# Kernel tuning notes

Hardware: AMD Instinct MI355X
Metric: run time of the kernel (lower is better)

Reference implementation:

```python
import jax, jax.numpy as jnp
import numpy as np

NUM_HEADS = 4

def setup_inputs() -> dict:
    key = jax.random.key(0)
    ks = jax.random.split(key, 5)
    B, N, C = 2, 4096, 256
    s = 0.02
    return {
        "x": jax.random.normal(ks[0], (B, N, C), dtype=jnp.float32),
        "qkv_w": jax.random.normal(ks[1], (3 * C, C), dtype=jnp.float32) * s,
        "qkv_b": jax.random.normal(ks[2], (3 * C,), dtype=jnp.float32) * s,
        "out_w": jax.random.normal(ks[3], (C, C), dtype=jnp.float32) * s,
        "out_b": jax.random.normal(ks[4], (C,), dtype=jnp.float32) * s,
    }

def reference(x, qkv_w, qkv_b, out_w, out_b):
    # x: [B, N, C]; manual multi-head self-attention (eval mode, dropout off)
    B, N, C = x.shape
    H = NUM_HEADS
    D = C // H
    qkv = x @ qkv_w.T + qkv_b                      # [B, N, 3C]
    qkv = qkv.reshape(B, N, 3, H, D)
    qkv = jnp.transpose(qkv, (2, 0, 3, 1, 4))      # [3, B, H, N, D]
    q, k, v = qkv[0], qkv[1], qkv[2]
    scale = D ** -0.5
    attn = jnp.einsum('bhnd,bhmd->bhnm', q, k) * scale  # [B, H, N, N]
    attn = jax.nn.softmax(attn, axis=-1)
    out = jnp.einsum('bhnm,bhmd->bhnd', attn, v)   # [B, H, N, D]
    out = jnp.transpose(out, (0, 2, 1, 3)).reshape(B, N, C)
    return out @ out_w.T + out_b
```

## Files before the change

kernel.cpp:

```cpp
#include <hip/hip_runtime.h>

typedef __bf16 bf16x8 __attribute__((ext_vector_type(8)));
typedef float f32x4 __attribute__((ext_vector_type(4)));

#define MFMA_BF16(a, b, c) __builtin_amdgcn_mfma_f32_16x16x32_bf16((a), (b), (c), 0, 0, 0)

#define C1 0.18033688f

static __device__ __forceinline__ unsigned short f2bf(float f) {
    unsigned int u = __float_as_uint(f);
    unsigned int r = (u + 0x7fffu + ((u >> 16) & 1u)) >> 16;
    return (unsigned short)r;
}
static __device__ __forceinline__ float bf2f(unsigned short us) {
    return __uint_as_float(((unsigned int)us) << 16);
}
static __device__ __forceinline__ float exp2_hw(float x) {
    float r;
    asm("v_exp_f32 %0, %1" : "=v"(r) : "v"(x));
    return r;
}
static __device__ __forceinline__ unsigned pack_rh(float a, float b) {
    return __byte_perm(__float_as_uint(a) + 0x8000u, __float_as_uint(b) + 0x8000u, 0x7632);
}
static __device__ __forceinline__ void gload16(const void* g, void* l) {
    __builtin_amdgcn_global_load_lds(
        (const __attribute__((address_space(1))) unsigned int*)g,
        (__attribute__((address_space(3))) unsigned int*)l, 16, 0, 0);
}

static __device__ __forceinline__ void conv_seg8(const void* src, unsigned short* dst, int n,
                                                 int lb, bool f32) {
    const int base = lb * 2048 + (int)threadIdx.x * 8;
    if (base < n) {
        if (f32) {
            const float4 u0 = *(const float4*)((const float*)src + base);
            const float4 u1 = *(const float4*)((const float*)src + base + 4);
            uint4 p;
            p.x = pack_rh(u0.x, u0.y);
            p.y = pack_rh(u0.z, u0.w);
            p.z = pack_rh(u1.x, u1.y);
            p.w = pack_rh(u1.z, u1.w);
            *(uint4*)(dst + base) = p;
        } else {
            *(uint4*)(dst + base) = *(const uint4*)((const unsigned short*)src + base);
        }
    }
}

__global__ __launch_bounds__(256) void convert_kernel(
    const void* __restrict__ x, const void* __restrict__ qw, const void* __restrict__ qb,
    const void* __restrict__ ow, const void* __restrict__ ob,
    unsigned short* __restrict__ xb, unsigned short* __restrict__ qwb,
    unsigned short* __restrict__ qbb, unsigned short* __restrict__ owb,
    unsigned short* __restrict__ obb, int* __restrict__ flag) {
    __shared__ int tot;
    if (threadIdx.x == 0) tot = 0;
    __syncthreads();
    {
        unsigned short v = ((const unsigned short*)x)[threadIdx.x];
        int e = (v >> 7) & 0xFF;
        if (e >= 195) atomicAdd(&tot, 1);
    }
    __syncthreads();
    const bool f32 = (tot >= 8);
    if (blockIdx.x == 0 && threadIdx.x == 0) flag[0] = f32 ? 1 : 0;

    const int bid = blockIdx.x;
    if (bid < 1024)       conv_seg8(x,  xb,  2097152, bid,        f32);
    else if (bid < 1120)  conv_seg8(qw, qwb, 196608,  bid - 1024, f32);
    else if (bid < 1121)  conv_seg8(qb, qbb, 768,     bid - 1120, f32);
    else if (bid < 1153)  conv_seg8(ow, owb, 65536,   bid - 1121, f32);
    else                  conv_seg8(ob, obb, 256,     bid - 1153, f32);
}

template <bool QKV>
__global__ __launch_bounds__(256) void gemm_kernel(
    const unsigned short* __restrict__ A, const unsigned short* __restrict__ W,
    const unsigned short* __restrict__ bias, unsigned short* __restrict__ Cb,
    float* __restrict__ Cf, const int* __restrict__ flag,
    unsigned short* __restrict__ Vt, int Nout) {
    constexpr int K = 256;
    __shared__ __align__(16) char sm[16384];

    const int tid = threadIdx.x;
    const int lane = tid & 63;
    const int wv = tid >> 6;
    const int m16 = lane & 15;
    const int quad = lane >> 4;
    const int bm = blockIdx.x * 64;
    const int bn = blockIdx.y * 64;

    int bgo[2], blo[2];
#pragma unroll
    for (int i = 0; i < 2; i++) {
        const int c = wv * 128 + i * 64 + lane;
        const int r = c >> 3, g = (c & 7) ^ (r & 7);
        bgo[i] = r * (K * 2) + g * 16;
        blo[i] = c * 16;
    }
    int bro[4][2];
#pragma unroll
    for (int t = 0; t < 4; t++)
#pragma unroll
        for (int ks = 0; ks < 2; ks++) {
            const int row = t * 16 + m16;
            bro[t][ks] = row * 64 + ((4 * ks + quad) ^ (m16 & 7)) * 8;
        }

    const char* bg = (const char*)(W + (size_t)bn * K);
    const unsigned short* ap = A + (size_t)(bm + wv * 16 + m16) * K + quad * 8;

#pragma unroll
    for (int i = 0; i < 2; i++) gload16(bg + bgo[i], sm + blo[i]);
    bf16x8 a0 = *(const bf16x8*)(ap);
    bf16x8 a1 = *(const bf16x8*)(ap + 32);

    f32x4 acc[4] = {};
#pragma unroll
    for (int kb = 0; kb < 4; kb++) {
        __syncthreads();
        const int cur = kb & 1;
        bf16x8 a0n, a1n;
        if (kb < 3) {
            bg += 128;
            char* Bdst = sm + (cur ^ 1) * 8192;
#pragma unroll
            for (int i = 0; i < 2; i++) gload16(bg + bgo[i], Bdst + blo[i]);
            a0n = *(const bf16x8*)(ap + (kb + 1) * 64);
            a1n = *(const bf16x8*)(ap + (kb + 1) * 64 + 32);
        }
        const unsigned short* Blds = (const unsigned short*)(sm + cur * 8192);
#pragma unroll
        for (int ks = 0; ks < 2; ks++) {
            const bf16x8 a = ks ? a1 : a0;
#pragma unroll
            for (int t = 0; t < 4; t++) {
                const bf16x8 b = *(const bf16x8*)(Blds + bro[t][ks]);
                acc[t] = MFMA_BF16(a, b, acc[t]);
            }
        }
        if (kb < 3) {
            a0 = a0n;
            a1 = a1n;
        }
    }

    if (QKV && bn >= 512) {
        __syncthreads();
        unsigned short* tr = (unsigned short*)sm;
        const int lr = wv * 16 + quad * 4;
#pragma unroll
        for (int t = 0; t < 4; t++) {
            const float bv = bf2f(bias[bn + t * 16 + m16]);
            uint2 w;
            w.x = pack_rh(acc[t][0] + bv, acc[t][1] + bv);
            w.y = pack_rh(acc[t][2] + bv, acc[t][3] + bv);
            *(uint2*)&tr[(t * 16 + m16) * 72 + lr] = w;
        }
        __syncthreads();
        const int d = tid >> 2;
        const int ch = (tid & 3) * 16;
        const uint4 o4a = *(const uint4*)&tr[d * 72 + ch];
        const uint4 o4b = *(const uint4*)&tr[d * 72 + ch + 8];
        const int hh = (bn - 512) >> 6;
        const int bb = bm >> 12, n0 = bm & 4095;
        const int nn = n0 + ch;
        const int kt = nn >> 7, koff = nn & 127;
        unsigned short* vdst =
            &Vt[(size_t)(((bb * 4 + hh) * 32 + kt) * 64 + d) * 128 + koff];
        *(uint4*)(vdst) = o4a;
        *(uint4*)(vdst + 8) = o4b;
        return;
    }

    const bool outf = (!QKV) && (flag != nullptr) && (*flag != 0);
    const int row0 = bm + wv * 16 + quad * 4;
#pragma unroll
    for (int t = 0; t < 4; t++) {
        const int col = bn + t * 16 + m16;
        const float bv = bf2f(bias[col]);
        float v[4];
#pragma unroll
        for (int r = 0; r < 4; r++) v[r] = acc[t][r] + bv;
        if (QKV) {
            const float sc = (col < 256) ? C1 : 1.0f;
#pragma unroll
            for (int r = 0; r < 4; r++)
                Cb[(size_t)(row0 + r) * 768 + col] = f2bf(v[r] * sc);
        } else {
            if (outf) {
#pragma unroll
                for (int r = 0; r < 4; r++) Cf[(size_t)(row0 + r) * Nout + col] = v[r];
            } else {
#pragma unroll
                for (int r = 0; r < 4; r++) Cb[(size_t)(row0 + r) * Nout + col] = f2bf(v[r]);
            }
        }
    }
}

#define ZERO_S(S)                                                     \
    do {                                                              \
        _Pragma("unroll") for (int mb = 0; mb < 2; mb++)              \
            _Pragma("unroll") for (int j = 0; j < 4; j++)             \
                S[mb][j] = (f32x4){0.f, 0.f, 0.f, 0.f};               \
    } while (0)

#define QKT(S, KBASE)                                                          \
    do {                                                                       \
        const unsigned short* Kb_ = (const unsigned short*)(KBASE);            \
        __builtin_amdgcn_s_setprio(1);                                         \
        _Pragma("unroll") for (int mb = 0; mb < 2; mb++)                       \
            _Pragma("unroll") for (int ks = 0; ks < 2; ks++) {                 \
                const bf16x8 ka_ = *(const bf16x8*)(Kb_ + kro[mb][ks]);        \
                _Pragma("unroll") for (int j = 0; j < 4; j++)                  \
                    S[mb][j] = MFMA_BF16(ka_, qf[j][ks], S[mb][j]);            \
            }                                                                  \
        __builtin_amdgcn_s_setprio(0);                                         \
    } while (0)

#define EXPP(S, PA)                                                            \
    do {                                                                       \
        _Pragma("unroll") for (int j = 0; j < 4; j++) {                        \
            const float e0 = exp2_hw(S[0][j][0]);                              \
            const float e1 = exp2_hw(S[0][j][1]);                              \
            const float e2 = exp2_hw(S[0][j][2]);                              \
            const float e3 = exp2_hw(S[0][j][3]);                              \
            const float e4 = exp2_hw(S[1][j][0]);                              \
            const float e5 = exp2_hw(S[1][j][1]);                              \
            const float e6 = exp2_hw(S[1][j][2]);                              \
            const float e7 = exp2_hw(S[1][j][3]);                              \
            uint4 pw_;                                                         \
            pw_.x = pack_rh(e0, e1);                                           \
            pw_.y = pack_rh(e2, e3);                                           \
            pw_.z = pack_rh(e4, e5);                                           \
            pw_.w = pack_rh(e6, e7);                                           \
            PA[j] = *(const bf16x8*)&pw_;                                      \
        }                                                                      \
    } while (0)

#define PVACC(PA, VBASE)                                                       \
    do {                                                                       \
        const unsigned short* Vb_ = (const unsigned short*)(VBASE);            \
        __builtin_amdgcn_s_setprio(1);                                         \
        _Pragma("unroll") for (int j = 0; j < 4; j++)                          \
            o1[j] = MFMA_BF16(PA[j], ones, o1[j]);                             \
        _Pragma("unroll") for (int t = 0; t < 4; t++) {                        \
            const uint2 va_ = *(const uint2*)(Vb_ + vroA[t]);                  \
            const uint2 vc_ = *(const uint2*)(Vb_ + (vroA[t] ^ 16));           \
            uint4 vv_;                                                         \
            vv_.x = va_.x;                                                     \
            vv_.y = va_.y;                                                     \
            vv_.z = vc_.x;                                                     \
            vv_.w = vc_.y;                                                     \
            const bf16x8 vb_ = *(const bf16x8*)&vv_;                           \
            _Pragma("unroll") for (int j = 0; j < 4; j++)                      \
                o[j][t] = MFMA_BF16(PA[j], vb_, o[j][t]);                      \
        }                                                                      \
        __builtin_amdgcn_s_setprio(0);                                         \
    } while (0)

#define GLK(DST)                                                               \
    {                                                                          \
        _Pragma("unroll") for (int i = 0; i < 4; i++)                          \
            gload16(kgn + kgo[i], (DST) + klo[i]);                             \
        kgn += 196608;                                                         \
    }
#define GLV(DST)                                                               \
    {                                                                          \
        _Pragma("unroll") for (int i = 0; i < 4; i++)                          \
            gload16(vgn + vgo[i], (DST) + vlo[i]);                             \
        vgn += 16384;                                                          \
    }

__global__ __launch_bounds__(256, 2) void attn_kernel(
    const unsigned short* __restrict__ qkv, const unsigned short* __restrict__ Vt,
    unsigned short* __restrict__ attn, int iters) {
    const int N = 4096, C3 = 768;
    __shared__ __align__(16) char sm[65536];

    const int tid = threadIdx.x;
    const int lane = tid & 63;
    const int wv = tid >> 6;
    const int m16 = lane & 15;
    const int quad = lane >> 4;

    const int bh = blockIdx.x & 7;
    const int qt = blockIdx.x >> 3;
    const int b = bh >> 2, h = bh & 3;

    bf16x8 qf[4][2];
#pragma unroll
    for (int j = 0; j < 4; j++)
#pragma unroll
        for (int ks = 0; ks < 2; ks++)
            qf[j][ks] = *(const bf16x8*)(qkv + ((size_t)b * N + qt * 64 + j * 16 + m16) * C3 +
                                         h * 64 + ks * 32 + quad * 8);

    uint4 ones_u;
    ones_u.x = ones_u.y = ones_u.z = ones_u.w = 0x3F803F80u;
    const bf16x8 ones = *(const bf16x8*)&ones_u;

    int kgo[4], vgo[4], klo[4], vlo[4];
#pragma unroll
    for (int i = 0; i < 4; i++) {
        const int c = i * 64 + lane;
        const int r = c >> 3, g = (c & 7) ^ (r & 7);
        kgo[i] = (wv * 32 + r) * 1536 + g * 16;
        klo[i] = c * 16;
        const int d = c >> 2, js = c & 3, jg = js ^ ((d >> 2) & 3);
        vgo[i] = d * 256 + wv * 64 + jg * 16;
        vlo[i] = c * 16;
    }
    int kro[2][2];
#pragma unroll
    for (int mb = 0; mb < 2; mb++)
#pragma unroll
        for (int ks = 0; ks < 2; ks++) {
            const int row = mb * 16 + m16;
            kro[mb][ks] = row * 64 + ((4 * ks + quad) ^ (m16 & 7)) * 8;
        }
    int vroA[4];
#pragma unroll
    for (int t = 0; t < 4; t++) {
        const int d = t * 16 + m16;
        const int c0 = (quad >> 1) ^ ((d >> 2) & 3);
        vroA[t] = d * 32 + c0 * 8 + (quad & 1) * 4;
    }

    char* Kreg0 = sm + wv * 8192;
    char* Vreg0 = sm + 32768 + wv * 8192;

    const char* kgp = (const char*)(qkv + (size_t)b * N * C3 + 256 + h * 64);
    const char* vgp = (const char*)(Vt + (size_t)bh * 262144);

#pragma unroll
    for (int i = 0; i < 4; i++) gload16(kgp + kgo[i], Kreg0 + klo[i]);
#pragma unroll
    for (int i = 0; i < 4; i++) gload16(vgp + vgo[i], Vreg0 + vlo[i]);
#pragma unroll
    for (int i = 0; i < 4; i++) gload16(kgp + 196608 + kgo[i], Kreg0 + 4096 + klo[i]);
#pragma unroll
    for (int i = 0; i < 4; i++) gload16(vgp + 16384 + vgo[i], Vreg0 + 4096 + vlo[i]);
    const char* kgn = kgp + 2 * 196608;
    const char* vgn = vgp + 2 * 16384;

    f32x4 o[4][4] = {};
    f32x4 o1[4] = {};
    f32x4 sA[2][4], sB[2][4];
    bf16x8 pa[4];

    asm volatile("s_waitcnt vmcnt(12)" ::: "memory");
    ZERO_S(sA);
    QKT(sA, Kreg0);

    for (int t2 = 0; t2 < 15; ++t2) {
        asm volatile("s_waitcnt vmcnt(4)" ::: "memory");
        GLK(Kreg0);
        ZERO_S(sB);
        QKT(sB, Kreg0 + 4096);
        EXPP(sA, pa);
        PVACC(pa, Vreg0);
        asm volatile("s_waitcnt lgkmcnt(0)" ::: "memory");
        GLV(Vreg0);

        asm volatile("s_waitcnt vmcnt(4)" ::: "memory");
        GLK(Kreg0 + 4096);
        ZERO_S(sA);
        QKT(sA, Kreg0);
        EXPP(sB, pa);
        PVACC(pa, Vreg0 + 4096);
        asm volatile("s_waitcnt lgkmcnt(0)" ::: "memory");
        GLV(Vreg0 + 4096);
    }
    asm volatile("s_waitcnt vmcnt(4)" ::: "memory");
    ZERO_S(sB);
    QKT(sB, Kreg0 + 4096);
    EXPP(sA, pa);
    PVACC(pa, Vreg0);
    asm volatile("s_waitcnt vmcnt(0)" ::: "memory");
    EXPP(sB, pa);
    PVACC(pa, Vreg0 + 4096);

    __syncthreads();
    float* Ored = (float*)sm;
    float* lsum = (float*)(sm + 16384);
    if (m16 == 0) {
#pragma unroll
        for (int j = 0; j < 4; j++)
#pragma unroll
            for (int r = 0; r < 4; r++)
                lsum[wv * 64 + j * 16 + quad * 4 + r] = o1[j][r];
    }
    const int row = tid >> 4;
    const int col = (tid & 15) * 4;
#pragma unroll
    for (int j = 0; j < 4; j++) {
#pragma unroll
        for (int t = 0; t < 4; t++)
#pragma unroll
            for (int r = 0; r < 4; r++)
                Ored[(wv * 16 + quad * 4 + r) * 64 + t * 16 + m16] = o[j][t][r];
        __syncthreads();
        f32x4 sum = *(f32x4*)&Ored[row * 64 + col];
        sum += *(f32x4*)&Ored[1024 + row * 64 + col];
        sum += *(f32x4*)&Ored[2048 + row * 64 + col];
        sum += *(f32x4*)&Ored[3072 + row * 64 + col];
        const float lq = lsum[j * 16 + row] + lsum[64 + j * 16 + row] +
                         lsum[128 + j * 16 + row] + lsum[192 + j * 16 + row];
        const int n = qt * 64 + j * 16 + row;
        const float inv = 1.0f / lq;
        uint2 w;
        w.x = pack_rh(sum[0] * inv, sum[1] * inv);
        w.y = pack_rh(sum[2] * inv, sum[3] * inv);
        *(uint2*)&attn[((size_t)b * N + n) * 256 + h * 64 + col] = w;
        __syncthreads();
    }
}

extern "C" void kernel_launch(void* const* d_in, const int* in_sizes, int n_in,
                              void* d_out, int out_size, void* d_ws, size_t ws_size,
                              hipStream_t stream) {
    const int B = 2, N = 4096, H = 4;
    const int M = B * N;

    char* wsb = (char*)d_ws;
    int* flag = (int*)wsb;
    unsigned short* xb      = (unsigned short*)(wsb + 64);
    unsigned short* qwb     = xb + 2097152;
    unsigned short* qbb     = qwb + 196608;
    unsigned short* owb     = qbb + 768;
    unsigned short* obb     = owb + 65536;
    unsigned short* qkv_ws  = obb + 256;
    unsigned short* Vt_ws   = qkv_ws + 6291456;
    unsigned short* attn_ws = Vt_ws + 2097152;

    convert_kernel<<<1154, 256, 0, stream>>>(d_in[0], d_in[1], d_in[2], d_in[3], d_in[4],
                                             xb, qwb, qbb, owb, obb, flag);

    gemm_kernel<true><<<dim3(M / 64, 768 / 64), 256, 0, stream>>>(
        xb, qwb, qbb, qkv_ws, nullptr, nullptr, Vt_ws, 768);

    attn_kernel<<<512, 256, 0, stream>>>(qkv_ws, Vt_ws, attn_ws, 32);

    gemm_kernel<false><<<dim3(M / 64, 256 / 64), 256, 0, stream>>>(
        attn_ws, owb, obb, (unsigned short*)d_out, (float*)d_out, flag, nullptr, 256);
}
```

Baseline: 133.7 us.

## Load K fragments directly from global into registers, drop K LDS staging

K tiles are now read straight from global memory into MFMA operand registers instead of being staged through shared memory with async loads and swizzled LDS reads. This halves the shared memory allocation (64KB to 32KB), which could allow more blocks per CU and removes the LDS write/read traffic for K. In exchange, the waits become vmcnt(0), so each iteration waits for all outstanding V and K loads, reducing how far loads can overlap compute. Global reads of K are also 16-byte per-lane loads with row stride 1536 bytes, so coalescing is weaker.

New measurement: 136.3 us. No clear change (+1.9%).

```diff
diff --git a/kernel.cpp b/kernel.cpp
--- a/kernel.cpp
+++ b/kernel.cpp
@@ -207,15 +207,21 @@
                 S[mb][j] = (f32x4){0.f, 0.f, 0.f, 0.f};               \
     } while (0)
 
-#define QKT(S, KBASE)                                                          \
+#define LDK(KP)                                                                \
     do {                                                                       \
-        const unsigned short* Kb_ = (const unsigned short*)(KBASE);            \
+        kf[0][0] = *(const bf16x8*)((KP));                                     \
+        kf[0][1] = *(const bf16x8*)((KP) + 64);                                \
+        kf[1][0] = *(const bf16x8*)((KP) + 24576);                             \
+        kf[1][1] = *(const bf16x8*)((KP) + 24576 + 64);                        \
+    } while (0)
+
+#define QKT(S)                                                                 \
+    do {                                                                       \
         __builtin_amdgcn_s_setprio(1);                                         \
         _Pragma("unroll") for (int mb = 0; mb < 2; mb++)                       \
             _Pragma("unroll") for (int ks = 0; ks < 2; ks++) {                 \
-                const bf16x8 ka_ = *(const bf16x8*)(Kb_ + kro[mb][ks]);        \
                 _Pragma("unroll") for (int j = 0; j < 4; j++)                  \
-                    S[mb][j] = MFMA_BF16(ka_, qf[j][ks], S[mb][j]);            \
+                    S[mb][j] = MFMA_BF16(kf[mb][ks], qf[j][ks], S[mb][j]);     \
             }                                                                  \
         __builtin_amdgcn_s_setprio(0);                                         \
     } while (0)
@@ -261,12 +267,6 @@
         __builtin_amdgcn_s_setprio(0);                                         \
     } while (0)
 
-#define GLK(DST)                                                               \
-    {                                                                          \
-        _Pragma("unroll") for (int i = 0; i < 4; i++)                          \
-            gload16(kgn + kgo[i], (DST) + klo[i]);                             \
-        kgn += 196608;                                                         \
-    }
 #define GLV(DST)                                                               \
     {                                                                          \
         _Pragma("unroll") for (int i = 0; i < 4; i++)                          \
@@ -278,7 +278,7 @@
     const unsigned short* __restrict__ qkv, const unsigned short* __restrict__ Vt,
     unsigned short* __restrict__ attn, int iters) {
     const int N = 4096, C3 = 768;
-    __shared__ __align__(16) char sm[65536];
+    __shared__ __align__(16) char sm[32768];
 
     const int tid = threadIdx.x;
     const int lane = tid & 63;
@@ -302,25 +302,14 @@
     ones_u.x = ones_u.y = ones_u.z = ones_u.w = 0x3F803F80u;
     const bf16x8 ones = *(const bf16x8*)&ones_u;
 
-    int kgo[4], vgo[4], klo[4], vlo[4];
+    int vgo[4], vlo[4];
 #pragma unroll
     for (int i = 0; i < 4; i++) {
         const int c = i * 64 + lane;
-        const int r = c >> 3, g = (c & 7) ^ (r & 7);
-        kgo[i] = (wv * 32 + r) * 1536 + g * 16;
-        klo[i] = c * 16;
         const int d = c >> 2, js = c & 3, jg = js ^ ((d >> 2) & 3);
         vgo[i] = d * 256 + wv * 64 + jg * 16;
         vlo[i] = c * 16;
     }
-    int kro[2][2];
-#pragma unroll
-    for (int mb = 0; mb < 2; mb++)
-#pragma unroll
-        for (int ks = 0; ks < 2; ks++) {
-            const int row = mb * 16 + m16;
-            kro[mb][ks] = row * 64 + ((4 * ks + quad) ^ (m16 & 7)) * 8;
-        }
     int vroA[4];
 #pragma unroll
     for (int t = 0; t < 4; t++) {
@@ -329,57 +318,52 @@
         vroA[t] = d * 32 + c0 * 8 + (quad & 1) * 4;
     }
 
-    char* Kreg0 = sm + wv * 8192;
-    char* Vreg0 = sm + 32768 + wv * 8192;
-
-    const char* kgp = (const char*)(qkv + (size_t)b * N * C3 + 256 + h * 64);
-    const char* vgp = (const char*)(Vt + (size_t)bh * 262144);
-
-#pragma unroll
-    for (int i = 0; i < 4; i++) gload16(kgp + kgo[i], Kreg0 + klo[i]);
-#pragma unroll
-    for (int i = 0; i < 4; i++) gload16(vgp + vgo[i], Vreg0 + vlo[i]);
-#pragma unroll
-    for (int i = 0; i < 4; i++) gload16(kgp + 196608 + kgo[i], Kreg0 + 4096 + klo[i]);
-#pragma unroll
-    for (int i = 0; i < 4; i++) gload16(vgp + 16384 + vgo[i], Vreg0 + 4096 + vlo[i]);
-    const char* kgn = kgp + 2 * 196608;
-    const char* vgn = vgp + 2 * 16384;
+    char* Vreg0 = sm + wv * 8192;
+
+    const char* kbn = (const char*)(qkv + (size_t)b * N * C3 + 256 + h * 64) +
+                      (size_t)(wv * 32 + m16) * 1536 + quad * 16;
+    const char* vgn = (const char*)(Vt + (size_t)bh * 262144);
 
     f32x4 o[4][4] = {};
     f32x4 o1[4] = {};
     f32x4 sA[2][4], sB[2][4];
     bf16x8 pa[4];
-
-    asm volatile("s_waitcnt vmcnt(12)" ::: "memory");
+    bf16x8 kf[2][2];
+
+    LDK(kbn);
+    GLV(Vreg0);
+    GLV(Vreg0 + 4096);
     ZERO_S(sA);
-    QKT(sA, Kreg0);
+    QKT(sA);
+    LDK(kbn + 196608);
+    kbn += 2 * 196608;
 
     for (int t2 = 0; t2 < 15; ++t2) {
-        asm volatile("s_waitcnt vmcnt(4)" ::: "memory");
-        GLK(Kreg0);
+        asm volatile("s_waitcnt vmcnt(0)" ::: "memory");
         ZERO_S(sB);
-        QKT(sB, Kreg0 + 4096);
+        QKT(sB);
         EXPP(sA, pa);
         PVACC(pa, Vreg0);
         asm volatile("s_waitcnt lgkmcnt(0)" ::: "memory");
         GLV(Vreg0);
-
-        asm volatile("s_waitcnt vmcnt(4)" ::: "memory");
-        GLK(Kreg0 + 4096);
+        LDK(kbn);
+        kbn += 196608;
+
+        asm volatile("s_waitcnt vmcnt(0)" ::: "memory");
         ZERO_S(sA);
-        QKT(sA, Kreg0);
+        QKT(sA);
         EXPP(sB, pa);
         PVACC(pa, Vreg0 + 4096);
         asm volatile("s_waitcnt lgkmcnt(0)" ::: "memory");
         GLV(Vreg0 + 4096);
-    }
-    asm volatile("s_waitcnt vmcnt(4)" ::: "memory");
+        LDK(kbn);
+        kbn += 196608;
+    }
+    asm volatile("s_waitcnt vmcnt(0)" ::: "memory");
     ZERO_S(sB);
-    QKT(sB, Kreg0 + 4096);
+    QKT(sB);
     EXPP(sA, pa);
     PVACC(pa, Vreg0);
-    asm volatile("s_waitcnt vmcnt(0)" ::: "memory");
     EXPP(sB, pa);
     PVACC(pa, Vreg0 + 4096);
 
```
